# Performance work log

Measured on AMD Instinct MI355X. Metric: run time of the kernel, lower is better.

The kernel has to match this reference:

```python
import jax, jax.numpy as jnp
import numpy as np

B, T, C = 2, 4096, 1024
H = 16            # n_head (== n_groups == n_kv_heads)
HD = C // H       # head_dim = 64
W = 256           # window_size
ROPE_BASE = 10000.0


def _rope(x):
    # x: (B, H, T, HD); rotate interleaved pairs with position along axis 2
    t = x.shape[2]
    inv_freq = 1.0 / (ROPE_BASE ** (jnp.arange(0, HD, 2, dtype=jnp.float32) / HD))  # (HD/2,)
    freqs = jnp.arange(t, dtype=jnp.float32)[:, None] * inv_freq[None, :]           # (T, HD/2)
    cos = jnp.cos(freqs)[None, None].astype(x.dtype)
    sin = jnp.sin(freqs)[None, None].astype(x.dtype)
    x1, x2 = x[..., 0::2], x[..., 1::2]
    o1 = x1 * cos - x2 * sin
    o2 = x1 * sin + x2 * cos
    return jnp.stack([o1, o2], axis=-1).reshape(x.shape)


def setup_inputs() -> dict:
    key = jax.random.key(0)
    ks = jax.random.split(key, 5)
    s = 1.0 / np.sqrt(C)
    return {
        "x": jax.random.normal(ks[0], (B, T, C), dtype=jnp.float32),
        "wq": jax.random.normal(ks[1], (C, C), dtype=jnp.float32) * s,
        "wk": jax.random.normal(ks[2], (C, C), dtype=jnp.float32) * s,
        "wv": jax.random.normal(ks[3], (C, C), dtype=jnp.float32) * s,
        "wo": jax.random.normal(ks[4], (C, C), dtype=jnp.float32) * s,
    }


def reference(x, wq, wk, wv, wo):
    # projections (Linear stores (out, in) -> x @ w.T)
    q = jnp.einsum('btc,oc->bto', x, wq).reshape(B, T, H, HD).transpose(0, 2, 1, 3)
    k = jnp.einsum('btc,oc->bto', x, wk).reshape(B, T, H, HD).transpose(0, 2, 1, 3)
    v = jnp.einsum('btc,oc->bto', x, wv).reshape(B, T, H, HD).transpose(0, 2, 1, 3)

    q = _rope(q)
    k = _rope(k)

    nW = T // W
    qw = q.reshape(B, H, nW, W, HD)
    kw = k.reshape(B, H, nW, W, HD)
    vw = v.reshape(B, H, nW, W, HD)

    scale = 1.0 / jnp.sqrt(jnp.asarray(HD, dtype=q.dtype))
    att = jnp.einsum('bhnqd,bhnkd->bhnqk', qw, kw) * scale   # per-window, no causal mask
    att = jax.nn.softmax(att, axis=-1)
    yw = jnp.einsum('bhnqk,bhnkd->bhnqd', att, vw)

    y = yw.reshape(B, H, T, HD).transpose(0, 2, 1, 3).reshape(B, T, C)
    return jnp.einsum('btc,oc->bto', y, wo)
```

## Files before the change

### kernel.cpp

```cpp
#include <hip/hip_runtime.h>
#include <math.h>

typedef float f32x4 __attribute__((ext_vector_type(4)));
typedef __bf16 bf16x8 __attribute__((ext_vector_type(8)));
typedef unsigned short ushort_t;

#define MFMA16(a, b, c) __builtin_amdgcn_mfma_f32_16x16x32_bf16((a), (b), (c), 0, 0, 0)

static __device__ __forceinline__ ushort_t f2bf(float f) {
  union { float f; unsigned u; } v; v.f = f;
  unsigned u = v.u;
  return (ushort_t)((u + 0x7FFFu + ((u >> 16) & 1u)) >> 16);
}
static __device__ __forceinline__ float bf2f(ushort_t h) {
  union { unsigned u; float f; } v; v.u = ((unsigned)h) << 16;
  return v.f;
}
static __device__ __forceinline__ void gl_lds16(const void* g, void* lds_uniform) {
  __builtin_amdgcn_global_load_lds(
      (const __attribute__((address_space(1))) unsigned int*)g,
      (__attribute__((address_space(3))) unsigned int*)lds_uniform, 16, 0, 0);
}

__global__ void prep(const float* __restrict__ x,
                     const float* __restrict__ wq, const float* __restrict__ wk,
                     const float* __restrict__ wv, const float* __restrict__ wo,
                     ushort_t* __restrict__ Xb, ushort_t* __restrict__ Wqb,
                     ushort_t* __restrict__ Wkb, ushort_t* __restrict__ Wvb,
                     ushort_t* __restrict__ Wob, float2* __restrict__ cs) {
  const int bid = blockIdx.x;
  if (bid < 12288) {
    const float* src;
    ushort_t* dst;
    int i;
    if (bid < 8192) {
      src = x; dst = Xb;
      i = bid * 256 + threadIdx.x;
    } else {
      const int wi = (bid - 8192) >> 10;
      src = (wi == 0) ? wq : (wi == 1) ? wk : (wi == 2) ? wv : wo;
      dst = (wi == 0) ? Wqb : (wi == 1) ? Wkb : (wi == 2) ? Wvb : Wob;
      i = ((bid - 8192) & 1023) * 256 + threadIdx.x;
    }
    f32x4 v = ((const f32x4*)src)[i];
    ushort4 o;
    o.x = f2bf(v.x); o.y = f2bf(v.y); o.z = f2bf(v.z); o.w = f2bf(v.w);
    ((ushort4*)dst)[i] = o;
  } else {
    int idx = (bid - 12288) * 256 + threadIdx.x;
    int pos = idx >> 5, i = idx & 31;
    double inv = exp2(-(double)i * 0.41524101186092029);
    double th = (double)pos * inv;
    double s, c;
    sincos(th, &s, &c);
    cs[idx] = make_float2((float)c, (float)s);
  }
}

template <int OUTBF>
__global__ __launch_bounds__(256) void gemm_nt(
    const ushort_t* __restrict__ A,
    const ushort_t* __restrict__ W0, const ushort_t* __restrict__ W1, const ushort_t* __restrict__ W2,
    void* __restrict__ C0, void* __restrict__ C1, void* __restrict__ C2,
    int K, int N) {
  __shared__ __align__(16) ushort_t As[128 * 64];
  __shared__ __align__(16) ushort_t Bs[128 * 64];
  const int z = blockIdx.z;
  const ushort_t* W = (z == 0) ? W0 : (z == 1 ? W1 : W2);
  void* Cv = (z == 0) ? C0 : (z == 1 ? C1 : C2);

  const int t = threadIdx.x;
  const int lane = t & 63;
  const int l15 = lane & 15;
  const int quad = lane >> 4;
  const int wave = t >> 6;
  const int wm = wave & 1, wn = wave >> 1;
  const int bm = blockIdx.x, bn = blockIdx.y;

  const int srow = t >> 3;
  const int schunk = (t & 7) ^ (srow & 7);
  const ushort_t* Ag = A + (size_t)(bm * 128 + srow) * K + schunk * 8;
  const ushort_t* Wg = W + (size_t)(bn * 128 + srow) * K + schunk * 8;
  char* AsB = (char*)As + (t & 192) * 16;
  char* BsB = (char*)Bs + (t & 192) * 16;
  const size_t rK = (size_t)32 * K;

  const f32x4 zero4 = {0.f, 0.f, 0.f, 0.f};
  f32x4 acc[4][4];
#pragma unroll
  for (int i = 0; i < 4; ++i)
#pragma unroll
    for (int j = 0; j < 4; ++j) acc[i][j] = zero4;

  for (int kt = 0; kt < K; kt += 64) {
#pragma unroll
    for (int p = 0; p < 4; ++p) {
      gl_lds16(Ag + p * rK + kt, AsB + p * 4096);
      gl_lds16(Wg + p * rK + kt, BsB + p * 4096);
    }
    __syncthreads();
#pragma unroll
    for (int ks = 0; ks < 2; ++ks) {
      bf16x8 af[4], bfr[4];
#pragma unroll
      for (int i = 0; i < 4; ++i) {
        const int r = wm * 64 + i * 16 + l15;
        af[i] = *(const bf16x8*)&As[r * 64 + (((ks * 4 + quad) ^ (r & 7)) * 8)];
      }
#pragma unroll
      for (int j = 0; j < 4; ++j) {
        const int r = wn * 64 + j * 16 + l15;
        bfr[j] = *(const bf16x8*)&Bs[r * 64 + (((ks * 4 + quad) ^ (r & 7)) * 8)];
      }
#pragma unroll
      for (int i = 0; i < 4; ++i)
#pragma unroll
        for (int j = 0; j < 4; ++j) acc[i][j] = MFMA16(af[i], bfr[j], acc[i][j]);
    }
    __syncthreads();
  }

  const int rbase = bm * 128 + wm * 64 + quad * 4;
  const int cbase = bn * 128 + wn * 64 + l15;
#pragma unroll
  for (int i = 0; i < 4; ++i)
#pragma unroll
    for (int j = 0; j < 4; ++j)
#pragma unroll
      for (int r = 0; r < 4; ++r) {
        size_t idx = (size_t)(rbase + i * 16 + r) * N + (cbase + j * 16);
        if (OUTBF)
          ((ushort_t*)Cv)[idx] = f2bf(acc[i][j][r]);
        else
          ((float*)Cv)[idx] = acc[i][j][r];
      }
}

static __device__ __forceinline__ void rope8(const ushort_t* __restrict__ g,
                                             ushort_t* __restrict__ lds,
                                             const float2* __restrict__ cs4, float scale) {
  uint4 raw = *(const uint4*)g;
  unsigned rw[4] = {raw.x, raw.y, raw.z, raw.w};
  ushort_t o[8];
#pragma unroll
  for (int m = 0; m < 4; ++m) {
    float x1 = bf2f((ushort_t)(rw[m] & 0xffffu));
    float x2 = bf2f((ushort_t)(rw[m] >> 16));
    float2 sc = cs4[m];
    o[2 * m]     = f2bf((x1 * sc.x - x2 * sc.y) * scale);
    o[2 * m + 1] = f2bf((x1 * sc.y + x2 * sc.x) * scale);
  }
  uint4 w;
  w.x = (unsigned)o[0] | ((unsigned)o[1] << 16);
  w.y = (unsigned)o[2] | ((unsigned)o[3] << 16);
  w.z = (unsigned)o[4] | ((unsigned)o[5] << 16);
  w.w = (unsigned)o[6] | ((unsigned)o[7] << 16);
  *(uint4*)lds = w;
}

__global__ __launch_bounds__(256, 2) void attn(
    const ushort_t* __restrict__ Qb, const ushort_t* __restrict__ Kb,
    const ushort_t* __restrict__ Vb, ushort_t* __restrict__ Yb,
    const float2* __restrict__ cs) {
  __shared__ __align__(16) ushort_t smem[27648];
  ushort_t* Qs = smem;
  ushort_t* Ks = smem + 9216;
  ushort_t* Vt = smem;
  ushort_t* Pc = smem + 16896;

  const int t = threadIdx.x;
  const int lane = t & 63, wave = t >> 6;
  const int l15 = lane & 15, quad = lane >> 4;
  const int win = blockIdx.x >> 1, slice = blockIdx.x & 1;
  const int h = blockIdx.y, b = blockIdx.z;
  const int kBase = win * 256, qBase = kBase + slice * 128;
  const size_t gbase = ((size_t)b * 4096) * 1024 + h * 64;

  const int sr = t >> 3;
  const int c0 = (t & 7) * 8;

#pragma unroll
  for (int p = 0; p < 4; ++p) {
    int r = p * 32 + sr;
    rope8(Qb + gbase + (size_t)(qBase + r) * 1024 + c0, Qs + r * 72 + c0,
          cs + (qBase + r) * 32 + (c0 >> 1), 0.125f);
  }
#pragma unroll
  for (int p = 0; p < 8; ++p) {
    int r = p * 32 + sr;
    rope8(Kb + gbase + (size_t)(kBase + r) * 1024 + c0, Ks + r * 72 + c0,
          cs + (kBase + r) * 32 + (c0 >> 1), 1.0f);
  }
  __syncthreads();

  const int qw = wave * 32;
  const f32x4 zero4 = {0.f, 0.f, 0.f, 0.f};
  f32x4 S[2][16];
#pragma unroll
  for (int i = 0; i < 2; ++i)
#pragma unroll
    for (int j = 0; j < 16; ++j) S[i][j] = zero4;
#pragma unroll
  for (int ks = 0; ks < 2; ++ks) {
    bf16x8 a0 = *(const bf16x8*)&Qs[(qw + l15) * 72 + ks * 32 + quad * 8];
    bf16x8 a1 = *(const bf16x8*)&Qs[(qw + 16 + l15) * 72 + ks * 32 + quad * 8];
#pragma unroll
    for (int j = 0; j < 16; ++j) {
      bf16x8 bk = *(const bf16x8*)&Ks[(j * 16 + l15) * 72 + ks * 32 + quad * 8];
      S[0][j] = MFMA16(a0, bk, S[0][j]);
      S[1][j] = MFMA16(a1, bk, S[1][j]);
    }
  }

  float linv[2][4];
#pragma unroll
  for (int i = 0; i < 2; ++i)
#pragma unroll
    for (int r = 0; r < 4; ++r) {
      float mx = S[i][0][r];
#pragma unroll
      for (int j = 1; j < 16; ++j) mx = fmaxf(mx, S[i][j][r]);
      mx = fmaxf(mx, __shfl_xor(mx, 1));
      mx = fmaxf(mx, __shfl_xor(mx, 2));
      mx = fmaxf(mx, __shfl_xor(mx, 4));
      mx = fmaxf(mx, __shfl_xor(mx, 8));
      float sum = 0.f;
#pragma unroll
      for (int j = 0; j < 16; ++j) {
        float e = __expf(S[i][j][r] - mx);
        S[i][j][r] = e;
        sum += e;
      }
      sum += __shfl_xor(sum, 1);
      sum += __shfl_xor(sum, 2);
      sum += __shfl_xor(sum, 4);
      sum += __shfl_xor(sum, 8);
      linv[i][r] = 1.0f / sum;
    }
  __syncthreads();

#pragma unroll
  for (int p = 0; p < 8; ++p) {
    int k = p * 32 + sr;
    uint4 raw = *(const uint4*)(Vb + gbase + (size_t)(kBase + k) * 1024 + c0);
    ushort_t vv[8];
    vv[0] = raw.x & 0xffffu; vv[1] = raw.x >> 16;
    vv[2] = raw.y & 0xffffu; vv[3] = raw.y >> 16;
    vv[4] = raw.z & 0xffffu; vv[5] = raw.z >> 16;
    vv[6] = raw.w & 0xffffu; vv[7] = raw.w >> 16;
#pragma unroll
    for (int e = 0; e < 8; ++e) {
      int ee = (e + (t & 7)) & 7;
      Vt[(c0 + ee) * 264 + k] = vv[ee];
    }
  }

  auto writeP = [&](int kc) {
#pragma unroll
    for (int i = 0; i < 2; ++i)
#pragma unroll
      for (int jj = 0; jj < 4; ++jj) {
        int j = kc * 4 + jj;
#pragma unroll
        for (int r = 0; r < 4; ++r)
          Pc[(qw + i * 16 + quad * 4 + r) * 72 + jj * 16 + l15] = f2bf(S[i][j][r]);
      }
  };

  writeP(0);
  __syncthreads();

  f32x4 O[2][4];
#pragma unroll
  for (int i = 0; i < 2; ++i)
#pragma unroll
    for (int jd = 0; jd < 4; ++jd) O[i][jd] = zero4;

  for (int kc = 0; kc < 4; ++kc) {
#pragma unroll
    for (int ks = 0; ks < 2; ++ks) {
      bf16x8 a0 = *(const bf16x8*)&Pc[(qw + l15) * 72 + ks * 32 + quad * 8];
      bf16x8 a1 = *(const bf16x8*)&Pc[(qw + 16 + l15) * 72 + ks * 32 + quad * 8];
#pragma unroll
      for (int jd = 0; jd < 4; ++jd) {
        bf16x8 bv = *(const bf16x8*)&Vt[(jd * 16 + l15) * 264 + kc * 64 + ks * 32 + quad * 8];
        O[0][jd] = MFMA16(a0, bv, O[0][jd]);
        O[1][jd] = MFMA16(a1, bv, O[1][jd]);
      }
    }
    if (kc < 3) {
      __syncthreads();
      writeP(kc + 1);
      __syncthreads();
    }
  }

#pragma unroll
  for (int i = 0; i < 2; ++i)
#pragma unroll
    for (int jd = 0; jd < 4; ++jd)
#pragma unroll
      for (int r = 0; r < 4; ++r) {
        int row = qBase + qw + i * 16 + quad * 4 + r;
        int col = jd * 16 + l15;
        Yb[gbase + (size_t)row * 1024 + col] = f2bf(O[i][jd][r] * linv[i][r]);
      }
}

extern "C" void kernel_launch(void* const* d_in, const int* in_sizes, int n_in,
                              void* d_out, int out_size, void* d_ws, size_t ws_size,
                              hipStream_t stream) {
  (void)in_sizes; (void)n_in; (void)out_size; (void)ws_size;
  const float* x  = (const float*)d_in[0];
  const float* wq = (const float*)d_in[1];
  const float* wk = (const float*)d_in[2];
  const float* wv = (const float*)d_in[3];
  const float* wo = (const float*)d_in[4];

  char* ws = (char*)d_ws;
  ushort_t* Xb  = (ushort_t*)(ws);
  ushort_t* Wqb = (ushort_t*)(ws + 16777216);
  ushort_t* Wkb = Wqb + 1048576;
  ushort_t* Wvb = Wkb + 1048576;
  ushort_t* Wob = Wvb + 1048576;
  ushort_t* Qb  = (ushort_t*)(ws + 25165824);
  ushort_t* Kb  = Qb + 8388608;
  ushort_t* Vb  = Kb + 8388608;
  ushort_t* Yb  = Vb + 8388608;
  float2*   cs  = (float2*)(ws + 92274688);

  prep<<<dim3(12800), dim3(256), 0, stream>>>(x, wq, wk, wv, wo,
                                              Xb, Wqb, Wkb, Wvb, Wob, cs);

  gemm_nt<1><<<dim3(64, 8, 3), dim3(256), 0, stream>>>(
      Xb, Wqb, Wkb, Wvb, (void*)Qb, (void*)Kb, (void*)Vb, 1024, 1024);

  attn<<<dim3(32, 16, 2), dim3(256), 0, stream>>>(Qb, Kb, Vb, Yb, cs);

  gemm_nt<0><<<dim3(64, 8, 1), dim3(256), 0, stream>>>(
      Yb, Wob, Wob, Wob, d_out, d_out, d_out, 1024, 1024);
}
```

Measured before the change: 211.6 us.

## Rewrite GEMM as 8-wave 256x128 tile with double-buffered LDS pipeline

Replaces the 4-wave 128x128 GEMM with an 8-wave kernel computing 256x128 tiles. LDS is double buffered, so the next K-slice is loaded by global_load_lds while MFMAs run on the current one. The MFMA work is split into two phases with explicit barriers, waitcnts, sched_barriers and setprio to interleave loads with compute. The goal is to hide global-memory latency and raise reuse per block. The cost is 96KB of LDS per block, which reduces occupancy, and a fragile hand-tuned synchronisation scheme.

```diff
diff --git a/kernel.cpp b/kernel.cpp
--- a/kernel.cpp
+++ b/kernel.cpp
@@ -58,32 +58,35 @@
 }
 
 template <int OUTBF>
-__global__ __launch_bounds__(256) void gemm_nt(
+__global__ __launch_bounds__(512, 2) void gemm8(
     const ushort_t* __restrict__ A,
     const ushort_t* __restrict__ W0, const ushort_t* __restrict__ W1, const ushort_t* __restrict__ W2,
     void* __restrict__ C0, void* __restrict__ C1, void* __restrict__ C2,
     int K, int N) {
-  __shared__ __align__(16) ushort_t As[128 * 64];
-  __shared__ __align__(16) ushort_t Bs[128 * 64];
+  __shared__ __align__(16) char smem[98304];
   const int z = blockIdx.z;
   const ushort_t* W = (z == 0) ? W0 : (z == 1 ? W1 : W2);
   void* Cv = (z == 0) ? C0 : (z == 1 ? C1 : C2);
 
   const int t = threadIdx.x;
   const int lane = t & 63;
-  const int l15 = lane & 15;
-  const int quad = lane >> 4;
+  const int l15 = lane & 15, quad = lane >> 4;
   const int wave = t >> 6;
-  const int wm = wave & 1, wn = wave >> 1;
+  const int wm = wave >> 1, wn = wave & 1;
   const int bm = blockIdx.x, bn = blockIdx.y;
 
-  const int srow = t >> 3;
-  const int schunk = (t & 7) ^ (srow & 7);
-  const ushort_t* Ag = A + (size_t)(bm * 128 + srow) * K + schunk * 8;
-  const ushort_t* Wg = W + (size_t)(bn * 128 + srow) * K + schunk * 8;
-  char* AsB = (char*)As + (t & 192) * 16;
-  char* BsB = (char*)Bs + (t & 192) * 16;
-  const size_t rK = (size_t)32 * K;
+  const int r0 = t >> 3;
+  const int gc = (t & 7) ^ (r0 & 7);
+  const ushort_t* Ag = A + (size_t)(bm * 256 + r0) * K + gc * 8;
+  const ushort_t* Wg = W + (size_t)(bn * 128 + r0) * K + gc * 8;
+  const size_t p64K = (size_t)64 * K;
+  char* ldsw = smem + wave * 1024;
+
+  const int sl0 = (quad ^ (l15 & 7)) * 16;
+  const int aoff = (wm * 64 + l15) * 128 + sl0;
+  const int boff = 65536 + (wn * 64 + l15) * 128 + sl0;
+
+  const int KT = K >> 6;
 
   const f32x4 zero4 = {0.f, 0.f, 0.f, 0.f};
   f32x4 acc[4][4];
@@ -92,47 +95,101 @@
 #pragma unroll
     for (int j = 0; j < 4; ++j) acc[i][j] = zero4;
 
-  for (int kt = 0; kt < K; kt += 64) {
-#pragma unroll
-    for (int p = 0; p < 4; ++p) {
-      gl_lds16(Ag + p * rK + kt, AsB + p * 4096);
-      gl_lds16(Wg + p * rK + kt, BsB + p * 4096);
-    }
-    __syncthreads();
-#pragma unroll
-    for (int ks = 0; ks < 2; ++ks) {
-      bf16x8 af[4], bfr[4];
-#pragma unroll
-      for (int i = 0; i < 4; ++i) {
-        const int r = wm * 64 + i * 16 + l15;
-        af[i] = *(const bf16x8*)&As[r * 64 + (((ks * 4 + quad) ^ (r & 7)) * 8)];
-      }
-#pragma unroll
-      for (int j = 0; j < 4; ++j) {
-        const int r = wn * 64 + j * 16 + l15;
-        bfr[j] = *(const bf16x8*)&Bs[r * 64 + (((ks * 4 + quad) ^ (r & 7)) * 8)];
-      }
-#pragma unroll
-      for (int i = 0; i < 4; ++i)
-#pragma unroll
-        for (int j = 0; j < 4; ++j) acc[i][j] = MFMA16(af[i], bfr[j], acc[i][j]);
-    }
-    __syncthreads();
-  }
-
-  const int rbase = bm * 128 + wm * 64 + quad * 4;
+  auto stA = [&](int buf, int p, int k0) {
+    gl_lds16(Ag + p64K * p + k0, ldsw + buf * 32768 + p * 8192);
+  };
+  auto stB = [&](int buf, int p, int k0) {
+    gl_lds16(Wg + p64K * p + k0, ldsw + 65536 + buf * 16384 + p * 8192);
+  };
+
+  stA(0, 0, 0); stA(0, 1, 0); stA(0, 2, 0); stA(0, 3, 0);
+  stB(0, 0, 0); stB(0, 1, 0);
+  stA(1, 0, 64); stA(1, 1, 64); stA(1, 2, 64); stA(1, 3, 64);
+  asm volatile("s_waitcnt vmcnt(4)" ::: "memory");
+  __builtin_amdgcn_s_barrier();
+
+  bf16x8 af[4][2], bfr[4][2];
+
+  for (int j = 0; j < KT; ++j) {
+    const int cb = j & 1, nb = cb ^ 1;
+    const char* Ab = smem + cb * 32768;
+    const char* Bb = smem + cb * 16384;
+
+#pragma unroll
+    for (int m = 0; m < 4; ++m) {
+      const int o = aoff + m * 2048;
+      af[m][0] = *(const bf16x8*)(Ab + o);
+      af[m][1] = *(const bf16x8*)(Ab + (o ^ 64));
+    }
+#pragma unroll
+    for (int n = 0; n < 2; ++n) {
+      const int o = boff + n * 2048;
+      bfr[n][0] = *(const bf16x8*)(Bb + o);
+      bfr[n][1] = *(const bf16x8*)(Bb + (o ^ 64));
+    }
+    if (j + 1 < KT) {
+      stB(nb, 0, (j + 1) * 64);
+      stB(nb, 1, (j + 1) * 64);
+    }
+    __builtin_amdgcn_s_barrier();
+    asm volatile("s_waitcnt lgkmcnt(0)" ::: "memory");
+    __builtin_amdgcn_sched_barrier(0);
+    __builtin_amdgcn_s_setprio(1);
+#pragma unroll
+    for (int m = 0; m < 4; ++m)
+#pragma unroll
+      for (int n = 0; n < 2; ++n) {
+        acc[m][n] = MFMA16(af[m][0], bfr[n][0], acc[m][n]);
+        acc[m][n] = MFMA16(af[m][1], bfr[n][1], acc[m][n]);
+      }
+    __builtin_amdgcn_s_setprio(0);
+    __builtin_amdgcn_sched_barrier(0);
+    __builtin_amdgcn_s_barrier();
+
+#pragma unroll
+    for (int n = 2; n < 4; ++n) {
+      const int o = boff + n * 2048;
+      bfr[n][0] = *(const bf16x8*)(Bb + o);
+      bfr[n][1] = *(const bf16x8*)(Bb + (o ^ 64));
+    }
+    if (j + 2 < KT) {
+      stA(cb, 0, (j + 2) * 64);
+      stA(cb, 1, (j + 2) * 64);
+      stA(cb, 2, (j + 2) * 64);
+      stA(cb, 3, (j + 2) * 64);
+      asm volatile("s_waitcnt vmcnt(4)" ::: "memory");
+    } else if (j + 1 < KT) {
+      asm volatile("s_waitcnt vmcnt(0)" ::: "memory");
+    }
+    __builtin_amdgcn_s_barrier();
+    asm volatile("s_waitcnt lgkmcnt(0)" ::: "memory");
+    __builtin_amdgcn_sched_barrier(0);
+    __builtin_amdgcn_s_setprio(1);
+#pragma unroll
+    for (int m = 0; m < 4; ++m)
+#pragma unroll
+      for (int n = 2; n < 4; ++n) {
+        acc[m][n] = MFMA16(af[m][0], bfr[n][0], acc[m][n]);
+        acc[m][n] = MFMA16(af[m][1], bfr[n][1], acc[m][n]);
+      }
+    __builtin_amdgcn_s_setprio(0);
+    __builtin_amdgcn_sched_barrier(0);
+    __builtin_amdgcn_s_barrier();
+  }
+
+  const int rbase = bm * 256 + wm * 64 + quad * 4;
   const int cbase = bn * 128 + wn * 64 + l15;
 #pragma unroll
-  for (int i = 0; i < 4; ++i)
-#pragma unroll
-    for (int j = 0; j < 4; ++j)
+  for (int m = 0; m < 4; ++m)
+#pragma unroll
+    for (int n = 0; n < 4; ++n)
 #pragma unroll
       for (int r = 0; r < 4; ++r) {
-        size_t idx = (size_t)(rbase + i * 16 + r) * N + (cbase + j * 16);
+        size_t idx = (size_t)(rbase + m * 16 + r) * N + (cbase + n * 16);
         if (OUTBF)
-          ((ushort_t*)Cv)[idx] = f2bf(acc[i][j][r]);
+          ((ushort_t*)Cv)[idx] = f2bf(acc[m][n][r]);
         else
-          ((float*)Cv)[idx] = acc[i][j][r];
+          ((float*)Cv)[idx] = acc[m][n][r];
       }
 }
 
@@ -332,11 +389,11 @@
   prep<<<dim3(12800), dim3(256), 0, stream>>>(x, wq, wk, wv, wo,
                                               Xb, Wqb, Wkb, Wvb, Wob, cs);
 
-  gemm_nt<1><<<dim3(64, 8, 3), dim3(256), 0, stream>>>(
+  gemm8<1><<<dim3(32, 8, 3), dim3(512), 0, stream>>>(
       Xb, Wqb, Wkb, Wvb, (void*)Qb, (void*)Kb, (void*)Vb, 1024, 1024);
 
   attn<<<dim3(32, 16, 2), dim3(256), 0, stream>>>(Qb, Kb, Vb, Yb, cs);
 
-  gemm_nt<0><<<dim3(64, 8, 1), dim3(256), 0, stream>>>(
+  gemm8<0><<<dim3(32, 8, 1), dim3(512), 0, stream>>>(
       Yb, Wob, Wob, Wob, d_out, d_out, d_out, 1024, 1024);
 }
```

After: 208.0 us. No clear change (-1.7%).

## Compute transposed scores with register-resident rope'd Q and drop per-chunk barriers

Applied to the files above, without the earlier changes.

The attention kernel now applies RoPE to Q straight into MFMA register fragments instead of staging Q in LDS, and computes S^T = K·Q^T so each lane owns a query column. Row max and sum then run mostly in registers, with only two cross-quad shuffles, and P is packed to bf16 in registers and written to LDS as 8-byte stores. V loads are issued before the barrier to overlap with the softmax. The two __syncthreads per P chunk are removed, since each wave only touches its own Pc rows. Shared memory shrinks and launch bounds go from 2 to 3 blocks per CU, which raises register pressure from holding the packed P and the prefetched V.

```diff
diff --git a/kernel.cpp b/kernel.cpp
--- a/kernel.cpp
+++ b/kernel.cpp
@@ -158,13 +158,30 @@
   *(uint4*)lds = w;
 }
 
-__global__ __launch_bounds__(256, 2) void attn(
+static __device__ __forceinline__ bf16x8 rope_frag(const ushort_t* __restrict__ g,
+                                                   const float2* __restrict__ cs4,
+                                                   float scale) {
+  uint4 raw = *(const uint4*)g;
+  unsigned rw[4] = {raw.x, raw.y, raw.z, raw.w};
+  union { unsigned u[4]; bf16x8 v; } out;
+#pragma unroll
+  for (int m = 0; m < 4; ++m) {
+    float x1 = bf2f((ushort_t)(rw[m] & 0xffffu));
+    float x2 = bf2f((ushort_t)(rw[m] >> 16));
+    float2 sc = cs4[m];
+    float o0 = (x1 * sc.x - x2 * sc.y) * scale;
+    float o1 = (x1 * sc.y + x2 * sc.x) * scale;
+    out.u[m] = (unsigned)f2bf(o0) | ((unsigned)f2bf(o1) << 16);
+  }
+  return out.v;
+}
+
+__global__ __launch_bounds__(256, 3) void attn(
     const ushort_t* __restrict__ Qb, const ushort_t* __restrict__ Kb,
     const ushort_t* __restrict__ Vb, ushort_t* __restrict__ Yb,
     const float2* __restrict__ cs) {
-  __shared__ __align__(16) ushort_t smem[27648];
-  ushort_t* Qs = smem;
-  ushort_t* Ks = smem + 9216;
+  __shared__ __align__(16) ushort_t smem[26112];
+  ushort_t* Ks = smem;
   ushort_t* Vt = smem;
   ushort_t* Pc = smem + 16896;
 
@@ -178,76 +195,88 @@
 
   const int sr = t >> 3;
   const int c0 = (t & 7) * 8;
-
-#pragma unroll
-  for (int p = 0; p < 4; ++p) {
-    int r = p * 32 + sr;
-    rope8(Qb + gbase + (size_t)(qBase + r) * 1024 + c0, Qs + r * 72 + c0,
-          cs + (qBase + r) * 32 + (c0 >> 1), 0.125f);
-  }
+  const int qw = wave * 32;
+
 #pragma unroll
   for (int p = 0; p < 8; ++p) {
     int r = p * 32 + sr;
     rope8(Kb + gbase + (size_t)(kBase + r) * 1024 + c0, Ks + r * 72 + c0,
-          cs + (kBase + r) * 32 + (c0 >> 1), 1.0f);
-  }
+          cs + (size_t)(kBase + r) * 32 + (c0 >> 1), 1.0f);
+  }
+
+  bf16x8 qf[2][2];
+#pragma unroll
+  for (int i = 0; i < 2; ++i)
+#pragma unroll
+    for (int ks = 0; ks < 2; ++ks) {
+      int row = qBase + qw + i * 16 + l15;
+      int col = ks * 32 + quad * 8;
+      qf[i][ks] = rope_frag(Qb + gbase + (size_t)row * 1024 + col,
+                            cs + (size_t)row * 32 + (col >> 1), 0.125f);
+    }
   __syncthreads();
 
-  const int qw = wave * 32;
   const f32x4 zero4 = {0.f, 0.f, 0.f, 0.f};
-  f32x4 S[2][16];
-#pragma unroll
-  for (int i = 0; i < 2; ++i)
-#pragma unroll
-    for (int j = 0; j < 16; ++j) S[i][j] = zero4;
-#pragma unroll
-  for (int ks = 0; ks < 2; ++ks) {
-    bf16x8 a0 = *(const bf16x8*)&Qs[(qw + l15) * 72 + ks * 32 + quad * 8];
-    bf16x8 a1 = *(const bf16x8*)&Qs[(qw + 16 + l15) * 72 + ks * 32 + quad * 8];
-#pragma unroll
-    for (int j = 0; j < 16; ++j) {
-      bf16x8 bk = *(const bf16x8*)&Ks[(j * 16 + l15) * 72 + ks * 32 + quad * 8];
-      S[0][j] = MFMA16(a0, bk, S[0][j]);
-      S[1][j] = MFMA16(a1, bk, S[1][j]);
-    }
-  }
-
-  float linv[2][4];
-#pragma unroll
-  for (int i = 0; i < 2; ++i)
-#pragma unroll
-    for (int r = 0; r < 4; ++r) {
-      float mx = S[i][0][r];
-#pragma unroll
-      for (int j = 1; j < 16; ++j) mx = fmaxf(mx, S[i][j][r]);
-      mx = fmaxf(mx, __shfl_xor(mx, 1));
-      mx = fmaxf(mx, __shfl_xor(mx, 2));
-      mx = fmaxf(mx, __shfl_xor(mx, 4));
-      mx = fmaxf(mx, __shfl_xor(mx, 8));
-      float sum = 0.f;
-#pragma unroll
-      for (int j = 0; j < 16; ++j) {
-        float e = __expf(S[i][j][r] - mx);
-        S[i][j][r] = e;
-        sum += e;
-      }
-      sum += __shfl_xor(sum, 1);
-      sum += __shfl_xor(sum, 2);
-      sum += __shfl_xor(sum, 4);
-      sum += __shfl_xor(sum, 8);
-      linv[i][r] = 1.0f / sum;
-    }
+  f32x4 ST[2][16];
+#pragma unroll
+  for (int i = 0; i < 2; ++i)
+#pragma unroll
+    for (int kt = 0; kt < 16; ++kt) ST[i][kt] = zero4;
+#pragma unroll
+  for (int ks = 0; ks < 2; ++ks)
+#pragma unroll
+    for (int kt = 0; kt < 16; ++kt) {
+      bf16x8 kf = *(const bf16x8*)&Ks[(kt * 16 + l15) * 72 + ks * 32 + quad * 8];
+      ST[0][kt] = MFMA16(kf, qf[0][ks], ST[0][kt]);
+      ST[1][kt] = MFMA16(kf, qf[1][ks], ST[1][kt]);
+    }
+
+  float mx[2], linv[2];
+#pragma unroll
+  for (int i = 0; i < 2; ++i) {
+    float m = ST[i][0][0];
+#pragma unroll
+    for (int kt = 0; kt < 16; ++kt)
+#pragma unroll
+      for (int r = 0; r < 4; ++r) m = fmaxf(m, ST[i][kt][r]);
+    m = fmaxf(m, __shfl_xor(m, 16));
+    m = fmaxf(m, __shfl_xor(m, 32));
+    mx[i] = m;
+  }
+  unsigned Pp[2][16][2];
+#pragma unroll
+  for (int i = 0; i < 2; ++i) {
+    float sum = 0.f;
+#pragma unroll
+    for (int kt = 0; kt < 16; ++kt) {
+      float e0 = __expf(ST[i][kt][0] - mx[i]);
+      float e1 = __expf(ST[i][kt][1] - mx[i]);
+      float e2 = __expf(ST[i][kt][2] - mx[i]);
+      float e3 = __expf(ST[i][kt][3] - mx[i]);
+      sum += (e0 + e1) + (e2 + e3);
+      Pp[i][kt][0] = (unsigned)f2bf(e0) | ((unsigned)f2bf(e1) << 16);
+      Pp[i][kt][1] = (unsigned)f2bf(e2) | ((unsigned)f2bf(e3) << 16);
+    }
+    sum += __shfl_xor(sum, 16);
+    sum += __shfl_xor(sum, 32);
+    linv[i] = 1.0f / sum;
+  }
+
+  uint4 vr[8];
+#pragma unroll
+  for (int p = 0; p < 8; ++p)
+    vr[p] = *(const uint4*)(Vb + gbase + (size_t)(kBase + p * 32 + sr) * 1024 + c0);
+
   __syncthreads();
 
 #pragma unroll
   for (int p = 0; p < 8; ++p) {
     int k = p * 32 + sr;
-    uint4 raw = *(const uint4*)(Vb + gbase + (size_t)(kBase + k) * 1024 + c0);
     ushort_t vv[8];
-    vv[0] = raw.x & 0xffffu; vv[1] = raw.x >> 16;
-    vv[2] = raw.y & 0xffffu; vv[3] = raw.y >> 16;
-    vv[4] = raw.z & 0xffffu; vv[5] = raw.z >> 16;
-    vv[6] = raw.w & 0xffffu; vv[7] = raw.w >> 16;
+    vv[0] = vr[p].x & 0xffffu; vv[1] = vr[p].x >> 16;
+    vv[2] = vr[p].y & 0xffffu; vv[3] = vr[p].y >> 16;
+    vv[4] = vr[p].z & 0xffffu; vv[5] = vr[p].z >> 16;
+    vv[6] = vr[p].w & 0xffffu; vv[7] = vr[p].w >> 16;
 #pragma unroll
     for (int e = 0; e < 8; ++e) {
       int ee = (e + (t & 7)) & 7;
@@ -259,11 +288,9 @@
 #pragma unroll
     for (int i = 0; i < 2; ++i)
 #pragma unroll
-      for (int jj = 0; jj < 4; ++jj) {
-        int j = kc * 4 + jj;
-#pragma unroll
-        for (int r = 0; r < 4; ++r)
-          Pc[(qw + i * 16 + quad * 4 + r) * 72 + jj * 16 + l15] = f2bf(S[i][j][r]);
+      for (int jt = 0; jt < 4; ++jt) {
+        uint2 w = make_uint2(Pp[i][kc * 4 + jt][0], Pp[i][kc * 4 + jt][1]);
+        *(uint2*)&Pc[(qw + i * 16 + l15) * 72 + jt * 16 + quad * 4] = w;
       }
   };
 
@@ -276,6 +303,7 @@
 #pragma unroll
     for (int jd = 0; jd < 4; ++jd) O[i][jd] = zero4;
 
+#pragma unroll
   for (int kc = 0; kc < 4; ++kc) {
 #pragma unroll
     for (int ks = 0; ks < 2; ++ks) {
@@ -288,13 +316,14 @@
         O[1][jd] = MFMA16(a1, bv, O[1][jd]);
       }
     }
-    if (kc < 3) {
-      __syncthreads();
-      writeP(kc + 1);
-      __syncthreads();
-    }
-  }
-
+    if (kc < 3) writeP(kc + 1);
+  }
+
+  float lv[2][4];
+#pragma unroll
+  for (int i = 0; i < 2; ++i)
+#pragma unroll
+    for (int r = 0; r < 4; ++r) lv[i][r] = __shfl(linv[i], quad * 4 + r);
 #pragma unroll
   for (int i = 0; i < 2; ++i)
 #pragma unroll
@@ -303,7 +332,7 @@
       for (int r = 0; r < 4; ++r) {
         int row = qBase + qw + i * 16 + quad * 4 + r;
         int col = jd * 16 + l15;
-        Yb[gbase + (size_t)row * 1024 + col] = f2bf(O[i][jd][r] * linv[i][r]);
+        Yb[gbase + (size_t)row * 1024 + col] = f2bf(O[i][jd][r] * lv[i][r]);
       }
 }
 
```

Result: slower. 233.6 us (+10.4%).
